# Performance work log

Measured on AMD Instinct MI355X. Metric: run time of the kernel, lower is better.

## Reference

```python
import jax, jax.numpy as jnp
import numpy as np

M, N, P, T = 8000, 63, 64, 5


def setup_inputs() -> dict:
    key = jax.random.key(0)
    ks = jax.random.split(key, 19)
    sn = (1.0 / N) ** 0.5
    sp = (1.0 / P) ** 0.5
    f32 = jnp.float32
    return {
        "A": jax.random.normal(ks[0], (1, M, N), f32),
        "b": jax.random.normal(ks[1], (1, M), f32),
        "c": jax.random.normal(ks[2], (1, N), f32),
        "theta1r": sn * jax.random.normal(ks[3], (P, N + 1), f32),
        "theta1c": sn * jax.random.normal(ks[4], (P, N + 1), f32),
        "theta2rr": sp * jax.random.normal(ks[5], (P, P), f32),
        "theta2rc": sp * jax.random.normal(ks[6], (P, P), f32),
        "theta2cr": sp * jax.random.normal(ks[7], (P, P), f32),
        "theta3rr": sp * jax.random.normal(ks[8], (P, P), f32),
        "theta3rc": sp * jax.random.normal(ks[9], (P, P), f32),
        "theta3cr": sp * jax.random.normal(ks[10], (P, P), f32),
        "theta4rr": sp * jax.random.normal(ks[11], (P,), f32),
        "theta4rc": sp * jax.random.normal(ks[12], (P,), f32),
        "theta4cr": sp * jax.random.normal(ks[13], (P,), f32),
        "theta6r": sp * jax.random.normal(ks[14], (P, P), f32),
        "theta6c": sp * jax.random.normal(ks[15], (P, P), f32),
        "theta7": sp * jax.random.normal(ks[16], (P, P), f32),
        "W8": 0.05 * jax.random.normal(ks[17], (2, 2 * P), f32),
        "b8": 0.05 * jax.random.normal(ks[18], (2,), f32),
        "z": 7,
    }


def reference(A, b, c, theta1r, theta1c, theta2rr, theta2rc, theta2cr,
              theta3rr, theta3rc, theta3cr, theta4rr, theta4rc, theta4cr,
              theta6r, theta6c, theta7, W8, b8, z):
    relu = jax.nn.relu
    m, n = A.shape[1], A.shape[2]
    p = theta1r.shape[0]
    # raw node features: row node v -> [A[v,:], b[v]]; column node m -> [c, 0]
    Fr_raw = jnp.concatenate([A[0], b[0][:, None]], axis=1)        # (m, n+1)
    fc_raw = jnp.concatenate([c[0], jnp.zeros((1,), A.dtype)])     # (n+1,)
    Fr = Fr_raw / jnp.linalg.norm(Fr_raw, axis=1, keepdims=True)   # f(v), v < m
    fc = fc_raw / jnp.linalg.norm(fc_raw)                          # f(m)
    # edge weights w(v,u) = f(v).f(u) are detached in the original (float(...data))
    Frd = jax.lax.stop_gradient(Fr)
    fcd = jax.lax.stop_gradient(fc)
    Wrr = Frd @ Frd.T                                              # (m, m)
    dg = jnp.diagonal(Wrr)
    srr_pos = relu(Wrr).sum(axis=1) - relu(dg)                     # sum over u != v
    srr_neg = relu(-Wrr).sum(axis=1) - relu(-dg)
    wrc = Frd @ fcd                                                # (m,) = w(v, m)
    # identity: sum_u relu(t4 * w_u) = relu(t4) * sum_u relu(w_u) + relu(-t4) * sum_u relu(-w_u)
    Srr = relu(theta4rr)[:, None] * srr_pos[None, :] + relu(-theta4rr)[:, None] * srr_neg[None, :]
    Src = relu(theta4rc)[:, None] * relu(wrc)[None, :] + relu(-theta4rc)[:, None] * relu(-wrc)[None, :]
    scr = relu(theta4cr) * relu(wrc).sum() + relu(-theta4cr) * relu(-wrc).sum()
    edge_r = theta3rr @ Srr + theta3rc @ Src                       # (p, m), constant over t
    edge_c = theta3cr @ scr                                        # (p,)
    fz = Fr[z]                                                     # z < m: row node feature
    t1r = theta1r @ fz                                             # (p,)
    t1c = theta1c @ fz
    # mu init (p, m+1) = [[Ab^T, c0^T]; 0]; split into row columns / column node
    mu_r0 = jnp.zeros((p, m), A.dtype).at[: n + 1].set(Fr_raw.T)
    mu_c0 = jnp.zeros((p,), A.dtype).at[: n + 1].set(fc_raw)

    def step(carry, _):
        mu_r, mu_c = carry
        # row nodes: term2rr uses old mu[:, v]; term2rc uses old mu[:, m]
        new_r = relu(t1r[:, None] + theta2rr @ mu_r + (theta2rc @ mu_c)[:, None] + edge_r)
        # column node updated last within a sweep -> sees updated row embeddings
        new_c = relu(t1c + theta2cr @ new_r.sum(axis=1) + edge_c)
        return (new_r, new_c), None

    (mu_r, mu_c), _ = jax.lax.scan(step, (mu_r0, mu_c0), None, length=T)
    term6 = theta6r @ mu_r.sum(axis=1) + theta6c @ mu_c            # (p,)
    term7 = theta7 @ mu_r[:, z]                                    # (p,)
    feat = jax.nn.sigmoid(jnp.concatenate([term6, term7]))         # (2p,)
    return (feat @ W8.T + b8)[None, :]                             # (1, 2)
```

## Files before the change

### kernel.cpp

```cpp
#include <hip/hip_runtime.h>
#include <math.h>

typedef __attribute__((ext_vector_type(8))) short short8;
typedef __attribute__((ext_vector_type(4))) float f32x4;

#define WS_SPART 0
#define WS_GPART 131072
#define WS_WPART 139264
#define WS_CPART 139520
#define WS_T1R   179520
#define WS_T1C   179584
#define WS_AL    179648
#define WS_BE    179712
#define WS_GA    179776
#define WS_DE    179840
#define WS_ECP   179904
#define WS_ECN   179968
#define WS_W     180032
#define WS_MUZ   180096
#define WS_WSUM  180160
#define WS_RNORM 180224
#define WS_E4    188416
#define WS_FH    220416
#define WS_FL    482560

__device__ __forceinline__ float waveReduceSum(float v) {
#pragma unroll
    for (int m = 32; m >= 1; m >>= 1) v += __shfl_xor(v, m, 64);
    return v;
}
__device__ __forceinline__ unsigned short f2bf(float f) {
    unsigned int u = __float_as_uint(f);
    unsigned int r = (u + 0x7fffu + ((u >> 16) & 1u)) >> 16;
    return (unsigned short)r;
}
__device__ __forceinline__ float bf2f(unsigned short h) {
    return __uint_as_float(((unsigned int)h) << 16);
}

__global__ __launch_bounds__(256) void k_fr(
    const float* __restrict__ A, const float* __restrict__ b, const float* __restrict__ c,
    const float* __restrict__ th1r, const float* __restrict__ th1c,
    const float* __restrict__ th2rc,
    const float* __restrict__ th3rr, const float* __restrict__ th3rc, const float* __restrict__ th3cr,
    const float* __restrict__ th4rr, const float* __restrict__ th4rc, const float* __restrict__ th4cr,
    const int* __restrict__ zp,
    unsigned short* __restrict__ Fh, unsigned short* __restrict__ Fl,
    float* __restrict__ ws)
{
    int tid = threadIdx.x, lane = tid & 63, wid = tid >> 6;

    if (blockIdx.x == 128) {
        __shared__ float fcraw[64], fz[64], sh4a[64], sh4b[64];
        int p = lane;
        int z = zp[0];
        float cv = (p < 63) ? c[p] : 0.f;
        fcraw[p] = cv;
        float av = (p < 63) ? A[z * 63 + p] : b[z];
        float s2 = waveReduceSum(av * av);
        fz[p] = av * rsqrtf(s2);
        __syncthreads();

        float t1 = 0.f, t2 = 0.f, w0 = 0.f;
#pragma unroll 8
        for (int k = 0; k < 64; k++) {
            t1 += th1r[p * 64 + k] * fz[k];
            t2 += th1c[p * 64 + k] * fz[k];
            w0 += th2rc[p * 64 + k] * fcraw[k];
        }
        ws[WS_T1R + p] = t1;
        ws[WS_T1C + p] = t2;
        ws[WS_W + p] = t1 + w0;

        sh4a[p] = th4rr[p];
        sh4b[p] = th4rc[p];
        __syncthreads();
        float a = 0.f, bb = 0.f, g = 0.f, d = 0.f;
#pragma unroll 8
        for (int k = 0; k < 64; k++) {
            float t4 = sh4a[k];
            a  += th3rr[p * 64 + k] * fmaxf(t4, 0.f);
            bb += th3rr[p * 64 + k] * fmaxf(-t4, 0.f);
            float t5 = sh4b[k];
            g  += th3rc[p * 64 + k] * fmaxf(t5, 0.f);
            d  += th3rc[p * 64 + k] * fmaxf(-t5, 0.f);
        }
        ws[WS_AL + p] = a; ws[WS_BE + p] = bb;
        ws[WS_GA + p] = g; ws[WS_DE + p] = d;
        __syncthreads();
        sh4a[p] = th4cr[p];
        __syncthreads();
        float e1 = 0.f, e2 = 0.f;
#pragma unroll 8
        for (int k = 0; k < 64; k++) {
            float t6 = sh4a[k];
            e1 += th3cr[p * 64 + k] * fmaxf(t6, 0.f);
            e2 += th3cr[p * 64 + k] * fmaxf(-t6, 0.f);
        }
        ws[WS_ECP + p] = e1; ws[WS_ECN + p] = e2;
        return;
    }

    __shared__ float gsh[64];
    __shared__ float wsh2[2];
    if (tid < 64) gsh[tid] = 0.f;
    if (tid < 2) wsh2[tid] = 0.f;
    __syncthreads();

    float cv = (lane < 63) ? c[lane] : 0.f;
    float cn2 = waveReduceSum(cv * cv);
    float fcnl = cv * rsqrtf(cn2);

    int gw = blockIdx.x * 4 + wid;
    float gl = 0.f, lp = 0.f, ln = 0.f;
    for (int r = gw; r < 8192; r += 512) {
        if (r < 8000) {
            float val = (lane < 63) ? A[r * 63 + lane] : b[r];
            float s2 = waveReduceSum(val * val);
            float f = val * rsqrtf(s2);
            unsigned short h = f2bf(f);
            Fh[r * 64 + lane] = h;
            Fl[r * 64 + lane] = f2bf(f - bf2f(h));
            gl += f;
            float w = waveReduceSum(f * fcnl);
            if (lane == 0) {
                ws[WS_RNORM + r] = sqrtf(s2);
                lp += fmaxf(w, 0.f); ln += fmaxf(-w, 0.f);
            }
        } else {
            Fh[r * 64 + lane] = 0;
            Fl[r * 64 + lane] = 0;
        }
    }
    atomicAdd(&gsh[lane], gl);
    if (lane == 0) { atomicAdd(&wsh2[0], lp); atomicAdd(&wsh2[1], ln); }
    __syncthreads();
    if (tid < 64) ws[WS_GPART + blockIdx.x * 64 + tid] = gsh[tid];
    if (tid == 64) ws[WS_WPART + blockIdx.x * 2 + 0] = wsh2[0];
    if (tid == 65) ws[WS_WPART + blockIdx.x * 2 + 1] = wsh2[1];
}

__global__ __launch_bounds__(256) void k_gram(
    const unsigned short* __restrict__ Fh, const unsigned short* __restrict__ Fl,
    float* __restrict__ ws)
{
    int tid = threadIdx.x, lane = tid & 63, wid = tid >> 6;
    int m = lane & 15, quad = lane >> 4;
    int vbase = blockIdx.x * 256 + wid * 64;

    short8 AH[8], AL[8];
#pragma unroll
    for (int pt = 0; pt < 4; pt++)
#pragma unroll
        for (int q = 0; q < 2; q++) {
            int off = (vbase + pt * 16 + m) * 64 + q * 32 + quad * 8;
            AH[pt * 2 + q] = *(const short8*)(Fh + off);
            AL[pt * 2 + q] = *(const short8*)(Fl + off);
        }
    float srr[16];
#pragma unroll
    for (int i = 0; i < 16; i++) srr[i] = 0.f;

    const int y = blockIdx.y;
    const int boff = m * 64 + quad * 8;
    short8 B0h[2], B0l[2], B1h[2], B1l[2];
#pragma unroll
    for (int q = 0; q < 2; q++) {
        B0h[q] = *(const short8*)(Fh + y * 16 * 64 + boff + q * 32);
        B0l[q] = *(const short8*)(Fl + y * 16 * 64 + boff + q * 32);
    }
#pragma unroll 1
    for (int ii = 0; ii < 16; ii++) {
        int jB = y + 32 * ii + 16;
#pragma unroll
        for (int q = 0; q < 2; q++) {
            B1h[q] = *(const short8*)(Fh + jB * 16 * 64 + boff + q * 32);
            B1l[q] = *(const short8*)(Fl + jB * 16 * 64 + boff + q * 32);
        }
#pragma unroll
        for (int pt = 0; pt < 4; pt++) {
            f32x4 a = {0.f, 0.f, 0.f, 0.f};
#pragma unroll
            for (int q = 0; q < 2; q++) {
                a = __builtin_amdgcn_mfma_f32_16x16x32_bf16(AH[pt*2+q], B0h[q], a, 0, 0, 0);
                a = __builtin_amdgcn_mfma_f32_16x16x32_bf16(AH[pt*2+q], B0l[q], a, 0, 0, 0);
                a = __builtin_amdgcn_mfma_f32_16x16x32_bf16(AL[pt*2+q], B0h[q], a, 0, 0, 0);
            }
#pragma unroll
            for (int r = 0; r < 4; r++) srr[pt*4+r] += fmaxf(a[r], 0.f);
        }
        if (ii < 15) {
            int jA = y + 32 * ii + 32;
#pragma unroll
            for (int q = 0; q < 2; q++) {
                B0h[q] = *(const short8*)(Fh + jA * 16 * 64 + boff + q * 32);
                B0l[q] = *(const short8*)(Fl + jA * 16 * 64 + boff + q * 32);
            }
        }
#pragma unroll
        for (int pt = 0; pt < 4; pt++) {
            f32x4 a = {0.f, 0.f, 0.f, 0.f};
#pragma unroll
            for (int q = 0; q < 2; q++) {
                a = __builtin_amdgcn_mfma_f32_16x16x32_bf16(AH[pt*2+q], B1h[q], a, 0, 0, 0);
                a = __builtin_amdgcn_mfma_f32_16x16x32_bf16(AH[pt*2+q], B1l[q], a, 0, 0, 0);
                a = __builtin_amdgcn_mfma_f32_16x16x32_bf16(AL[pt*2+q], B1h[q], a, 0, 0, 0);
            }
#pragma unroll
            for (int r = 0; r < 4; r++) srr[pt*4+r] += fmaxf(a[r], 0.f);
        }
    }
#pragma unroll
    for (int pt = 0; pt < 4; pt++)
#pragma unroll
        for (int r = 0; r < 4; r++) {
            float s = srr[pt * 4 + r];
#pragma unroll
            for (int mm = 8; mm >= 1; mm >>= 1) s += __shfl_xor(s, mm, 64);
            if (m == 0)
                ws[WS_SPART + y * 8192 + vbase + pt * 16 + quad * 4 + r] = s;
        }
}

__global__ __launch_bounds__(64) void k_e4(
    const float* __restrict__ c, float* __restrict__ ws,
    unsigned short* __restrict__ MH, unsigned short* __restrict__ ML)
{
    __shared__ float fcnS[64], gS[64];
    int lane = threadIdx.x;
    float cv = (lane < 63) ? c[lane] : 0.f;
    float cn2 = waveReduceSum(cv * cv);
    fcnS[lane] = cv * rsqrtf(cn2);

    float gv = 0.f;
#pragma unroll 8
    for (int blk = 0; blk < 128; blk++) gv += ws[WS_GPART + blk * 64 + lane];
    gS[lane] = gv;

    float wp = ws[WS_WPART + lane * 2] + ws[WS_WPART + (lane + 64) * 2];
    float wn = ws[WS_WPART + lane * 2 + 1] + ws[WS_WPART + (lane + 64) * 2 + 1];
    wp = waveReduceSum(wp); wn = waveReduceSum(wn);
    if (lane == 0) { ws[WS_WSUM] = wp; ws[WS_WSUM + 1] = wn; }
    __syncthreads();

    int v = blockIdx.x * 64 + lane;
    float spv = 0.f;
#pragma unroll
    for (int y = 0; y < 16; y++) spv += ws[WS_SPART + y * 8192 + v];

    float fr[64];
#pragma unroll
    for (int i = 0; i < 8; i++) {
        short8 h8 = *(const short8*)(MH + v * 64 + i * 8);
        short8 l8 = *(const short8*)(ML + v * 64 + i * 8);
#pragma unroll
        for (int j = 0; j < 8; j++)
            fr[i * 8 + j] = bf2f((unsigned short)h8[j]) + bf2f((unsigned short)l8[j]);
    }
    float dw = 0.f, dg = 0.f;
#pragma unroll 8
    for (int k = 0; k < 64; k++) { dw += fr[k] * fcnS[k]; dg += fr[k] * gS[k]; }
    float4 e;
    e.x = spv - 1.0f;
    e.y = spv - dg;
    e.z = fmaxf(dw, 0.f);
    e.w = fmaxf(-dw, 0.f);
    *(float4*)(ws + WS_E4 + v * 4) = e;

    float rnv = ws[WS_RNORM + v];
#pragma unroll
    for (int i = 0; i < 16; i++) {
        ushort4 h4, l4;
        float x0 = fr[4*i] * rnv, x1 = fr[4*i+1] * rnv;
        float x2 = fr[4*i+2] * rnv, x3 = fr[4*i+3] * rnv;
        h4.x = f2bf(x0); l4.x = f2bf(x0 - bf2f(h4.x));
        h4.y = f2bf(x1); l4.y = f2bf(x1 - bf2f(h4.y));
        h4.z = f2bf(x2); l4.z = f2bf(x2 - bf2f(h4.z));
        h4.w = f2bf(x3); l4.w = f2bf(x3 - bf2f(h4.w));
        *(ushort4*)(MH + v * 64 + 4 * i) = h4;
        *(ushort4*)(ML + v * 64 + 4 * i) = l4;
    }
}

__global__ __launch_bounds__(256) void k_iter(
    const float* __restrict__ th2rr, const float* __restrict__ th2cr,
    const float* __restrict__ th2rc, const int* __restrict__ zp,
    float* __restrict__ ws, unsigned short* __restrict__ MH,
    unsigned short* __restrict__ ML, int t)
{
    __shared__ __align__(16) float wsh[64], alS[64], beS[64], gaS[64], deS[64];
    __shared__ float red[256], Ssh[64], ysh[64], colp[256];
    int tid = threadIdx.x, lane = tid & 63, wid = tid >> 6;
    int m = lane & 15, quad = lane >> 4;
    int v = (blockIdx.x * 4 + wid) * 16 + m;

    if (tid < 64) {
        alS[tid] = ws[WS_AL + tid]; beS[tid] = ws[WS_BE + tid];
        gaS[tid] = ws[WS_GA + tid]; deS[tid] = ws[WS_DE + tid];
    }
    if (t == 0) {
        if (tid >= 64 && tid < 128) wsh[tid - 64] = ws[WS_W + tid - 64];
        __syncthreads();
    } else {
        int p = lane;
        float s = 0.f;
        for (int blk = wid; blk < 125; blk += 4)
            s += ws[WS_CPART + (t - 1) * 8000 + blk * 64 + p];
        red[wid * 64 + p] = s;
        __syncthreads();
        if (tid < 64) Ssh[tid] = red[tid] + red[64 + tid] + red[128 + tid] + red[192 + tid];
        __syncthreads();
        if (tid < 64) {
            float acc = ws[WS_T1C + tid] + ws[WS_WSUM] * ws[WS_ECP + tid]
                      + ws[WS_WSUM + 1] * ws[WS_ECN + tid];
#pragma unroll 8
            for (int k = 0; k < 64; k++) acc += th2cr[tid * 64 + k] * Ssh[k];
            ysh[tid] = fmaxf(acc, 0.f);
        }
        __syncthreads();
        if (tid < 64) {
            float w = ws[WS_T1R + tid];
#pragma unroll 8
            for (int k = 0; k < 64; k++) w += th2rc[tid * 64 + k] * ysh[k];
            wsh[tid] = w;
        }
        __syncthreads();
    }

    short8 RH[8], RL[8];
#pragma unroll
    for (int pt = 0; pt < 4; pt++)
#pragma unroll
        for (int q = 0; q < 2; q++) {
            const float* rp = th2rr + (pt * 16 + m) * 64 + q * 32 + quad * 8;
            short8 H, L;
#pragma unroll
            for (int j = 0; j < 8; j++) {
                float f = rp[j];
                unsigned short h = f2bf(f);
                H[j] = (short)h;
                L[j] = (short)f2bf(f - bf2f(h));
            }
            RH[pt * 2 + q] = H; RL[pt * 2 + q] = L;
        }
    short8 BH[2], BL[2];
#pragma unroll
    for (int q = 0; q < 2; q++) {
        BH[q] = *(const short8*)(MH + v * 64 + q * 32 + quad * 8);
        BL[q] = *(const short8*)(ML + v * 64 + q * 32 + quad * 8);
    }
    float4 e = *(const float4*)(ws + WS_E4 + v * 4);
    int z = zp[0];

#pragma unroll
    for (int pt = 0; pt < 4; pt++) {
        f32x4 a = {0.f, 0.f, 0.f, 0.f};
#pragma unroll
        for (int q = 0; q < 2; q++) {
            a = __builtin_amdgcn_mfma_f32_16x16x32_bf16(RH[pt*2+q], BH[q], a, 0, 0, 0);
            a = __builtin_amdgcn_mfma_f32_16x16x32_bf16(RH[pt*2+q], BL[q], a, 0, 0, 0);
            a = __builtin_amdgcn_mfma_f32_16x16x32_bf16(RL[pt*2+q], BH[q], a, 0, 0, 0);
        }
        int pbase = pt * 16 + quad * 4;
        float4 w4 = *(const float4*)(wsh + pbase);
        float4 a4 = *(const float4*)(alS + pbase);
        float4 b4 = *(const float4*)(beS + pbase);
        float4 g4 = *(const float4*)(gaS + pbase);
        float4 d4 = *(const float4*)(deS + pbase);
        float v0 = fmaxf(a[0] + w4.x + a4.x*e.x + b4.x*e.y + g4.x*e.z + d4.x*e.w, 0.f);
        float v1 = fmaxf(a[1] + w4.y + a4.y*e.x + b4.y*e.y + g4.y*e.z + d4.y*e.w, 0.f);
        float v2 = fmaxf(a[2] + w4.z + a4.z*e.x + b4.z*e.y + g4.z*e.z + d4.z*e.w, 0.f);
        float v3 = fmaxf(a[3] + w4.w + a4.w*e.x + b4.w*e.y + g4.w*e.z + d4.w*e.w, 0.f);
        ushort4 h4, l4;
        h4.x = f2bf(v0); l4.x = f2bf(v0 - bf2f(h4.x));
        h4.y = f2bf(v1); l4.y = f2bf(v1 - bf2f(h4.y));
        h4.z = f2bf(v2); l4.z = f2bf(v2 - bf2f(h4.z));
        h4.w = f2bf(v3); l4.w = f2bf(v3 - bf2f(h4.w));
        *(ushort4*)(MH + v * 64 + pbase) = h4;
        *(ushort4*)(ML + v * 64 + pbase) = l4;
        float c0 = v0, c1 = v1, c2 = v2, c3 = v3;
#pragma unroll
        for (int mm = 1; mm < 16; mm <<= 1) {
            c0 += __shfl_xor(c0, mm, 64);
            c1 += __shfl_xor(c1, mm, 64);
            c2 += __shfl_xor(c2, mm, 64);
            c3 += __shfl_xor(c3, mm, 64);
        }
        if (m == 0) {
            colp[wid * 64 + pbase + 0] = c0;
            colp[wid * 64 + pbase + 1] = c1;
            colp[wid * 64 + pbase + 2] = c2;
            colp[wid * 64 + pbase + 3] = c3;
        }
        if (t == 4 && v == z) {
            float4 o; o.x = v0; o.y = v1; o.z = v2; o.w = v3;
            *(float4*)(ws + WS_MUZ + pbase) = o;
        }
    }
    __syncthreads();
    if (tid < 64)
        ws[WS_CPART + t * 8000 + blockIdx.x * 64 + tid] =
            colp[tid] + colp[64 + tid] + colp[128 + tid] + colp[192 + tid];
}

__global__ __launch_bounds__(64) void k_head(
    const float* __restrict__ th2cr,
    const float* __restrict__ th6r, const float* __restrict__ th6c, const float* __restrict__ th7,
    const float* __restrict__ W8, const float* __restrict__ b8,
    float* __restrict__ ws, float* __restrict__ out)
{
    int p = threadIdx.x;
    __shared__ float S[64], y[64], feat[128];
    float s = 0.f;
#pragma unroll 8
    for (int blk = 0; blk < 125; blk++) s += ws[WS_CPART + 4 * 8000 + blk * 64 + p];
    S[p] = s;
    __syncthreads();
    float acc = ws[WS_T1C + p] + ws[WS_WSUM] * ws[WS_ECP + p]
              + ws[WS_WSUM + 1] * ws[WS_ECN + p];
#pragma unroll 8
    for (int k = 0; k < 64; k++) acc += th2cr[p * 64 + k] * S[k];
    y[p] = fmaxf(acc, 0.f);
    __syncthreads();
    float t6 = 0.f, t7 = 0.f;
#pragma unroll 8
    for (int k = 0; k < 64; k++) {
        t6 += th6r[p * 64 + k] * S[k] + th6c[p * 64 + k] * y[k];
        t7 += th7[p * 64 + k] * ws[WS_MUZ + k];
    }
    feat[p] = 1.f / (1.f + expf(-t6));
    feat[64 + p] = 1.f / (1.f + expf(-t7));
    __syncthreads();
    if (p < 2) {
        float o = b8[p];
        for (int i = 0; i < 128; i++) o += W8[p * 128 + i] * feat[i];
        out[p] = o;
    }
}

extern "C" void kernel_launch(void* const* d_in, const int* in_sizes, int n_in,
                              void* d_out, int out_size, void* d_ws, size_t ws_size,
                              hipStream_t stream) {
    (void)in_sizes; (void)n_in; (void)out_size; (void)ws_size;
    const float* A     = (const float*)d_in[0];
    const float* b     = (const float*)d_in[1];
    const float* c     = (const float*)d_in[2];
    const float* th1r  = (const float*)d_in[3];
    const float* th1c  = (const float*)d_in[4];
    const float* th2rr = (const float*)d_in[5];
    const float* th2rc = (const float*)d_in[6];
    const float* th2cr = (const float*)d_in[7];
    const float* th3rr = (const float*)d_in[8];
    const float* th3rc = (const float*)d_in[9];
    const float* th3cr = (const float*)d_in[10];
    const float* th4rr = (const float*)d_in[11];
    const float* th4rc = (const float*)d_in[12];
    const float* th4cr = (const float*)d_in[13];
    const float* th6r  = (const float*)d_in[14];
    const float* th6c  = (const float*)d_in[15];
    const float* th7   = (const float*)d_in[16];
    const float* W8    = (const float*)d_in[17];
    const float* b8    = (const float*)d_in[18];
    const int*   zp    = (const int*)d_in[19];
    float* ws  = (float*)d_ws;
    float* out = (float*)d_out;
    unsigned short* Fh = (unsigned short*)(ws + WS_FH);
    unsigned short* Fl = (unsigned short*)(ws + WS_FL);

    k_fr<<<129, 256, 0, stream>>>(A, b, c, th1r, th1c, th2rc, th3rr, th3rc, th3cr,
                                  th4rr, th4rc, th4cr, zp, Fh, Fl, ws);
    k_gram<<<dim3(32, 16), 256, 0, stream>>>(Fh, Fl, ws);
    k_e4<<<125, 64, 0, stream>>>(c, ws, Fh, Fl);
    for (int t = 0; t < 5; t++)
        k_iter<<<125, 256, 0, stream>>>(th2rr, th2cr, th2rc, zp, ws, Fh, Fl, t);
    k_head<<<1, 64, 0, stream>>>(th2cr, th6r, th6c, th7, W8, b8, ws, out);
}
```

Baseline: 240.2 us.

## Widen gram grid, parallelize e4/head reductions, precompute theta2rr bf16 splits

The gram kernel grid doubles along y, so each block walks half as many column tiles and the partial-sum buffer grows to match. k_e4 and k_head move to 256 threads and split their reductions across waves, and k_e4 processes one row per wave with lane-level reductions. theta2rr is split into bf16 hi/lo once in k_fr instead of in every k_iter block. k_iter's small 64x64 matvecs now spread across all four waves. The aim is to raise parallelism in the small serial kernels and remove redundant conversion work, at the cost of more partial-sum traffic.

```diff
diff --git a/kernel.cpp b/kernel.cpp
--- a/kernel.cpp
+++ b/kernel.cpp
@@ -5,24 +5,26 @@
 typedef __attribute__((ext_vector_type(4))) float f32x4;
 
 #define WS_SPART 0
-#define WS_GPART 131072
-#define WS_WPART 139264
-#define WS_CPART 139520
-#define WS_T1R   179520
-#define WS_T1C   179584
-#define WS_AL    179648
-#define WS_BE    179712
-#define WS_GA    179776
-#define WS_DE    179840
-#define WS_ECP   179904
-#define WS_ECN   179968
-#define WS_W     180032
-#define WS_MUZ   180096
-#define WS_WSUM  180160
-#define WS_RNORM 180224
-#define WS_E4    188416
-#define WS_FH    220416
-#define WS_FL    482560
+#define WS_GPART 262144
+#define WS_WPART 270336
+#define WS_CPART 270592
+#define WS_T1R   310592
+#define WS_T1C   310656
+#define WS_AL    310720
+#define WS_BE    310784
+#define WS_GA    310848
+#define WS_DE    310912
+#define WS_ECP   310976
+#define WS_ECN   311040
+#define WS_W     311104
+#define WS_MUZ   311168
+#define WS_WSUM  311232
+#define WS_RNORM 311296
+#define WS_R2H   319488
+#define WS_R2L   321536
+#define WS_E4    323584
+#define WS_FH    355584
+#define WS_FL    617728
 
 __device__ __forceinline__ float waveReduceSum(float v) {
 #pragma unroll
@@ -41,11 +43,12 @@
 __global__ __launch_bounds__(256) void k_fr(
     const float* __restrict__ A, const float* __restrict__ b, const float* __restrict__ c,
     const float* __restrict__ th1r, const float* __restrict__ th1c,
-    const float* __restrict__ th2rc,
+    const float* __restrict__ th2rr, const float* __restrict__ th2rc,
     const float* __restrict__ th3rr, const float* __restrict__ th3rc, const float* __restrict__ th3cr,
     const float* __restrict__ th4rr, const float* __restrict__ th4rc, const float* __restrict__ th4cr,
     const int* __restrict__ zp,
     unsigned short* __restrict__ Fh, unsigned short* __restrict__ Fl,
+    unsigned short* __restrict__ R2H, unsigned short* __restrict__ R2L,
     float* __restrict__ ws)
 {
     int tid = threadIdx.x, lane = tid & 63, wid = tid >> 6;
@@ -98,6 +101,15 @@
             e2 += th3cr[p * 64 + k] * fmaxf(-t6, 0.f);
         }
         ws[WS_ECP + p] = e1; ws[WS_ECN + p] = e2;
+
+#pragma unroll
+        for (int i = 0; i < 16; i++) {
+            int idx = tid * 16 + i;
+            float f = th2rr[idx];
+            unsigned short h = f2bf(f);
+            R2H[idx] = h;
+            R2L[idx] = f2bf(f - bf2f(h));
+        }
         return;
     }
 
@@ -170,12 +182,12 @@
         B0l[q] = *(const short8*)(Fl + y * 16 * 64 + boff + q * 32);
     }
 #pragma unroll 1
-    for (int ii = 0; ii < 16; ii++) {
-        int jB = y + 32 * ii + 16;
+    for (int ii = 0; ii < 8; ii++) {
+        int tB1 = y + 64 * ii + 32;
 #pragma unroll
         for (int q = 0; q < 2; q++) {
-            B1h[q] = *(const short8*)(Fh + jB * 16 * 64 + boff + q * 32);
-            B1l[q] = *(const short8*)(Fl + jB * 16 * 64 + boff + q * 32);
+            B1h[q] = *(const short8*)(Fh + tB1 * 16 * 64 + boff + q * 32);
+            B1l[q] = *(const short8*)(Fl + tB1 * 16 * 64 + boff + q * 32);
         }
 #pragma unroll
         for (int pt = 0; pt < 4; pt++) {
@@ -189,12 +201,12 @@
 #pragma unroll
             for (int r = 0; r < 4; r++) srr[pt*4+r] += fmaxf(a[r], 0.f);
         }
-        if (ii < 15) {
-            int jA = y + 32 * ii + 32;
+        if (ii < 7) {
+            int tB0 = y + 64 * ii + 64;
 #pragma unroll
             for (int q = 0; q < 2; q++) {
-                B0h[q] = *(const short8*)(Fh + jA * 16 * 64 + boff + q * 32);
-                B0l[q] = *(const short8*)(Fl + jA * 16 * 64 + boff + q * 32);
+                B0h[q] = *(const short8*)(Fh + tB0 * 16 * 64 + boff + q * 32);
+                B0l[q] = *(const short8*)(Fl + tB0 * 16 * 64 + boff + q * 32);
             }
         }
 #pragma unroll
@@ -222,71 +234,76 @@
         }
 }
 
-__global__ __launch_bounds__(64) void k_e4(
+__global__ __launch_bounds__(256) void k_e4(
     const float* __restrict__ c, float* __restrict__ ws,
     unsigned short* __restrict__ MH, unsigned short* __restrict__ ML)
 {
-    __shared__ float fcnS[64], gS[64];
-    int lane = threadIdx.x;
+    __shared__ float fcnS[64], gS[64], sprow[64], red[256];
+    int tid = threadIdx.x, lane = tid & 63, wid = tid >> 6;
+
     float cv = (lane < 63) ? c[lane] : 0.f;
     float cn2 = waveReduceSum(cv * cv);
-    fcnS[lane] = cv * rsqrtf(cn2);
+    if (wid == 0) fcnS[lane] = cv * rsqrtf(cn2);
 
     float gv = 0.f;
 #pragma unroll 8
-    for (int blk = 0; blk < 128; blk++) gv += ws[WS_GPART + blk * 64 + lane];
-    gS[lane] = gv;
-
-    float wp = ws[WS_WPART + lane * 2] + ws[WS_WPART + (lane + 64) * 2];
-    float wn = ws[WS_WPART + lane * 2 + 1] + ws[WS_WPART + (lane + 64) * 2 + 1];
-    wp = waveReduceSum(wp); wn = waveReduceSum(wn);
-    if (lane == 0) { ws[WS_WSUM] = wp; ws[WS_WSUM + 1] = wn; }
-    __syncthreads();
-
-    int v = blockIdx.x * 64 + lane;
-    float spv = 0.f;
-#pragma unroll
-    for (int y = 0; y < 16; y++) spv += ws[WS_SPART + y * 8192 + v];
-
-    float fr[64];
-#pragma unroll
-    for (int i = 0; i < 8; i++) {
-        short8 h8 = *(const short8*)(MH + v * 64 + i * 8);
-        short8 l8 = *(const short8*)(ML + v * 64 + i * 8);
-#pragma unroll
-        for (int j = 0; j < 8; j++)
-            fr[i * 8 + j] = bf2f((unsigned short)h8[j]) + bf2f((unsigned short)l8[j]);
-    }
-    float dw = 0.f, dg = 0.f;
-#pragma unroll 8
-    for (int k = 0; k < 64; k++) { dw += fr[k] * fcnS[k]; dg += fr[k] * gS[k]; }
-    float4 e;
-    e.x = spv - 1.0f;
-    e.y = spv - dg;
-    e.z = fmaxf(dw, 0.f);
-    e.w = fmaxf(-dw, 0.f);
-    *(float4*)(ws + WS_E4 + v * 4) = e;
-
-    float rnv = ws[WS_RNORM + v];
-#pragma unroll
-    for (int i = 0; i < 16; i++) {
-        ushort4 h4, l4;
-        float x0 = fr[4*i] * rnv, x1 = fr[4*i+1] * rnv;
-        float x2 = fr[4*i+2] * rnv, x3 = fr[4*i+3] * rnv;
-        h4.x = f2bf(x0); l4.x = f2bf(x0 - bf2f(h4.x));
-        h4.y = f2bf(x1); l4.y = f2bf(x1 - bf2f(h4.y));
-        h4.z = f2bf(x2); l4.z = f2bf(x2 - bf2f(h4.z));
-        h4.w = f2bf(x3); l4.w = f2bf(x3 - bf2f(h4.w));
-        *(ushort4*)(MH + v * 64 + 4 * i) = h4;
-        *(ushort4*)(ML + v * 64 + 4 * i) = l4;
+    for (int blk = wid * 32; blk < wid * 32 + 32; blk++)
+        gv += ws[WS_GPART + blk * 64 + lane];
+    red[tid] = gv;
+    __syncthreads();
+    if (tid < 64) gS[tid] = red[tid] + red[64 + tid] + red[128 + tid] + red[192 + tid];
+    if (wid == 1) {
+        float wp = ws[WS_WPART + lane * 2] + ws[WS_WPART + (lane + 64) * 2];
+        wp = waveReduceSum(wp);
+        if (lane == 0) ws[WS_WSUM] = wp;
+    }
+    if (wid == 2) {
+        float wn = ws[WS_WPART + lane * 2 + 1] + ws[WS_WPART + (lane + 64) * 2 + 1];
+        wn = waveReduceSum(wn);
+        if (lane == 0) ws[WS_WSUM + 1] = wn;
+    }
+    int v0 = blockIdx.x * 64;
+    float sv = 0.f;
+#pragma unroll
+    for (int y = wid * 8; y < wid * 8 + 8; y++)
+        sv += ws[WS_SPART + y * 8192 + v0 + lane];
+    __syncthreads();
+    red[tid] = sv;
+    __syncthreads();
+    if (tid < 64) sprow[tid] = red[tid] + red[64 + tid] + red[128 + tid] + red[192 + tid];
+    __syncthreads();
+
+    for (int i2 = 0; i2 < 16; i2++) {
+        int i = wid * 16 + i2;
+        int v = v0 + i;
+        unsigned short fh = MH[v * 64 + lane];
+        unsigned short fl = ML[v * 64 + lane];
+        float fr = bf2f(fh) + bf2f(fl);
+        float dw = waveReduceSum(fr * fcnS[lane]);
+        float dg = waveReduceSum(fr * gS[lane]);
+        if (lane == 0) {
+            float spv = sprow[i];
+            float4 e;
+            e.x = spv - 1.0f;
+            e.y = spv - dg;
+            e.z = fmaxf(dw, 0.f);
+            e.w = fmaxf(-dw, 0.f);
+            *(float4*)(ws + WS_E4 + v * 4) = e;
+        }
+        float rnv = ws[WS_RNORM + v];
+        float x = fr * rnv;
+        unsigned short h = f2bf(x);
+        MH[v * 64 + lane] = h;
+        ML[v * 64 + lane] = f2bf(x - bf2f(h));
     }
 }
 
 __global__ __launch_bounds__(256) void k_iter(
-    const float* __restrict__ th2rr, const float* __restrict__ th2cr,
-    const float* __restrict__ th2rc, const int* __restrict__ zp,
-    float* __restrict__ ws, unsigned short* __restrict__ MH,
-    unsigned short* __restrict__ ML, int t)
+    const float* __restrict__ th2cr, const float* __restrict__ th2rc,
+    const int* __restrict__ zp, float* __restrict__ ws,
+    unsigned short* __restrict__ MH, unsigned short* __restrict__ ML,
+    const unsigned short* __restrict__ R2H, const unsigned short* __restrict__ R2L,
+    int t)
 {
     __shared__ __align__(16) float wsh[64], alS[64], beS[64], gaS[64], deS[64];
     __shared__ float red[256], Ssh[64], ysh[64], colp[256];
@@ -302,27 +319,43 @@
         if (tid >= 64 && tid < 128) wsh[tid - 64] = ws[WS_W + tid - 64];
         __syncthreads();
     } else {
-        int p = lane;
         float s = 0.f;
         for (int blk = wid; blk < 125; blk += 4)
-            s += ws[WS_CPART + (t - 1) * 8000 + blk * 64 + p];
-        red[wid * 64 + p] = s;
+            s += ws[WS_CPART + (t - 1) * 8000 + blk * 64 + lane];
+        red[tid] = s;
         __syncthreads();
         if (tid < 64) Ssh[tid] = red[tid] + red[64 + tid] + red[128 + tid] + red[192 + tid];
         __syncthreads();
-        if (tid < 64) {
-            float acc = ws[WS_T1C + tid] + ws[WS_WSUM] * ws[WS_ECP + tid]
-                      + ws[WS_WSUM + 1] * ws[WS_ECN + tid];
-#pragma unroll 8
-            for (int k = 0; k < 64; k++) acc += th2cr[tid * 64 + k] * Ssh[k];
-            ysh[tid] = fmaxf(acc, 0.f);
-        }
-        __syncthreads();
-        if (tid < 64) {
-            float w = ws[WS_T1R + tid];
-#pragma unroll 8
-            for (int k = 0; k < 64; k++) w += th2rc[tid * 64 + k] * ysh[k];
-            wsh[tid] = w;
+        {
+            int p = wid * 16 + m;
+            float acc = 0.f;
+            const float4* rowp = (const float4*)(th2cr + p * 64 + quad * 16);
+#pragma unroll
+            for (int kk = 0; kk < 4; kk++) {
+                float4 r4 = rowp[kk];
+                acc += r4.x * Ssh[quad * 16 + 4 * kk]     + r4.y * Ssh[quad * 16 + 4 * kk + 1]
+                     + r4.z * Ssh[quad * 16 + 4 * kk + 2] + r4.w * Ssh[quad * 16 + 4 * kk + 3];
+            }
+            acc += __shfl_xor(acc, 16, 64);
+            acc += __shfl_xor(acc, 32, 64);
+            if (quad == 0)
+                ysh[p] = fmaxf(acc + ws[WS_T1C + p] + ws[WS_WSUM] * ws[WS_ECP + p]
+                               + ws[WS_WSUM + 1] * ws[WS_ECN + p], 0.f);
+        }
+        __syncthreads();
+        {
+            int p = wid * 16 + m;
+            float acc = 0.f;
+            const float4* rowp = (const float4*)(th2rc + p * 64 + quad * 16);
+#pragma unroll
+            for (int kk = 0; kk < 4; kk++) {
+                float4 r4 = rowp[kk];
+                acc += r4.x * ysh[quad * 16 + 4 * kk]     + r4.y * ysh[quad * 16 + 4 * kk + 1]
+                     + r4.z * ysh[quad * 16 + 4 * kk + 2] + r4.w * ysh[quad * 16 + 4 * kk + 3];
+            }
+            acc += __shfl_xor(acc, 16, 64);
+            acc += __shfl_xor(acc, 32, 64);
+            if (quad == 0) wsh[p] = acc + ws[WS_T1R + p];
         }
         __syncthreads();
     }
@@ -332,16 +365,9 @@
     for (int pt = 0; pt < 4; pt++)
 #pragma unroll
         for (int q = 0; q < 2; q++) {
-            const float* rp = th2rr + (pt * 16 + m) * 64 + q * 32 + quad * 8;
-            short8 H, L;
-#pragma unroll
-            for (int j = 0; j < 8; j++) {
-                float f = rp[j];
-                unsigned short h = f2bf(f);
-                H[j] = (short)h;
-                L[j] = (short)f2bf(f - bf2f(h));
-            }
-            RH[pt * 2 + q] = H; RL[pt * 2 + q] = L;
+            int off = (pt * 16 + m) * 64 + q * 32 + quad * 8;
+            RH[pt * 2 + q] = *(const short8*)(R2H + off);
+            RL[pt * 2 + q] = *(const short8*)(R2L + off);
         }
     short8 BH[2], BL[2];
 #pragma unroll
@@ -403,33 +429,40 @@
             colp[tid] + colp[64 + tid] + colp[128 + tid] + colp[192 + tid];
 }
 
-__global__ __launch_bounds__(64) void k_head(
+__global__ __launch_bounds__(256) void k_head(
     const float* __restrict__ th2cr,
     const float* __restrict__ th6r, const float* __restrict__ th6c, const float* __restrict__ th7,
     const float* __restrict__ W8, const float* __restrict__ b8,
     float* __restrict__ ws, float* __restrict__ out)
 {
-    int p = threadIdx.x;
-    __shared__ float S[64], y[64], feat[128];
+    int tid = threadIdx.x, lane = tid & 63, wid = tid >> 6;
+    __shared__ float red[256], S[64], y[64], feat[128];
     float s = 0.f;
+    for (int blk = wid; blk < 125; blk += 4)
+        s += ws[WS_CPART + 4 * 8000 + blk * 64 + lane];
+    red[tid] = s;
+    __syncthreads();
+    if (tid < 64) S[tid] = red[tid] + red[64 + tid] + red[128 + tid] + red[192 + tid];
+    __syncthreads();
+    int p = tid;
+    if (p < 64) {
+        float acc = ws[WS_T1C + p] + ws[WS_WSUM] * ws[WS_ECP + p]
+                  + ws[WS_WSUM + 1] * ws[WS_ECN + p];
 #pragma unroll 8
-    for (int blk = 0; blk < 125; blk++) s += ws[WS_CPART + 4 * 8000 + blk * 64 + p];
-    S[p] = s;
-    __syncthreads();
-    float acc = ws[WS_T1C + p] + ws[WS_WSUM] * ws[WS_ECP + p]
-              + ws[WS_WSUM + 1] * ws[WS_ECN + p];
+        for (int k = 0; k < 64; k++) acc += th2cr[p * 64 + k] * S[k];
+        y[p] = fmaxf(acc, 0.f);
+    }
+    __syncthreads();
+    if (p < 64) {
+        float t6 = 0.f, t7 = 0.f;
 #pragma unroll 8
-    for (int k = 0; k < 64; k++) acc += th2cr[p * 64 + k] * S[k];
-    y[p] = fmaxf(acc, 0.f);
-    __syncthreads();
-    float t6 = 0.f, t7 = 0.f;
-#pragma unroll 8
-    for (int k = 0; k < 64; k++) {
-        t6 += th6r[p * 64 + k] * S[k] + th6c[p * 64 + k] * y[k];
-        t7 += th7[p * 64 + k] * ws[WS_MUZ + k];
-    }
-    feat[p] = 1.f / (1.f + expf(-t6));
-    feat[64 + p] = 1.f / (1.f + expf(-t7));
+        for (int k = 0; k < 64; k++) {
+            t6 += th6r[p * 64 + k] * S[k] + th6c[p * 64 + k] * y[k];
+            t7 += th7[p * 64 + k] * ws[WS_MUZ + k];
+        }
+        feat[p] = 1.f / (1.f + expf(-t6));
+        feat[64 + p] = 1.f / (1.f + expf(-t7));
+    }
     __syncthreads();
     if (p < 2) {
         float o = b8[p];
@@ -464,14 +497,16 @@
     const int*   zp    = (const int*)d_in[19];
     float* ws  = (float*)d_ws;
     float* out = (float*)d_out;
-    unsigned short* Fh = (unsigned short*)(ws + WS_FH);
-    unsigned short* Fl = (unsigned short*)(ws + WS_FL);
-
-    k_fr<<<129, 256, 0, stream>>>(A, b, c, th1r, th1c, th2rc, th3rr, th3rc, th3cr,
-                                  th4rr, th4rc, th4cr, zp, Fh, Fl, ws);
-    k_gram<<<dim3(32, 16), 256, 0, stream>>>(Fh, Fl, ws);
-    k_e4<<<125, 64, 0, stream>>>(c, ws, Fh, Fl);
+    unsigned short* Fh  = (unsigned short*)(ws + WS_FH);
+    unsigned short* Fl  = (unsigned short*)(ws + WS_FL);
+    unsigned short* R2H = (unsigned short*)(ws + WS_R2H);
+    unsigned short* R2L = (unsigned short*)(ws + WS_R2L);
+
+    k_fr<<<129, 256, 0, stream>>>(A, b, c, th1r, th1c, th2rr, th2rc, th3rr, th3rc,
+                                  th3cr, th4rr, th4rc, th4cr, zp, Fh, Fl, R2H, R2L, ws);
+    k_gram<<<dim3(32, 32), 256, 0, stream>>>(Fh, Fl, ws);
+    k_e4<<<125, 256, 0, stream>>>(c, ws, Fh, Fl);
     for (int t = 0; t < 5; t++)
-        k_iter<<<125, 256, 0, stream>>>(th2rr, th2cr, th2rc, zp, ws, Fh, Fl, t);
-    k_head<<<1, 64, 0, stream>>>(th2cr, th6r, th6c, th7, W8, b8, ws, out);
-}
+        k_iter<<<125, 256, 0, stream>>>(th2cr, th2rc, zp, ws, Fh, Fl, R2H, R2L, t);
+    k_head<<<1, 256, 0, stream>>>(th2cr, th6r, th6c, th7, W8, b8, ws, out);
+}
```

Measured after the change: 238.1 us. Within noise of the previous version (-0.9%).
